# Kernel tuning notes

Measured on AMD Instinct MI355X. Metric: run time of the kernel, lower is better.

The kernel has to match this reference:

```python
import jax, jax.numpy as jnp
import numpy as np

IN_DIM = 128
OUT_DIM = 128
HEADS = 4
HEAD_DIM = OUT_DIM // HEADS
N_NODES = 50000
N_EDGES = 800000
NEG_SLOPE = 0.2
LN_EPS = 1e-5


def setup_inputs() -> dict:
    key = jax.random.key(0)
    ks = jax.random.split(key, 10)
    x = jax.random.normal(ks[0], (N_NODES, IN_DIM), dtype=jnp.float32)
    edge_index = jax.random.randint(ks[1], (2, N_EDGES), 0, N_NODES, dtype=jnp.int64)
    s = 1.0 / np.sqrt(IN_DIM)
    W_l = jax.random.normal(ks[2], (IN_DIM, HEADS * HEAD_DIM), dtype=jnp.float32) * s
    b_l = jnp.zeros((HEADS * HEAD_DIM,), dtype=jnp.float32)
    W_r = jax.random.normal(ks[3], (IN_DIM, HEADS * HEAD_DIM), dtype=jnp.float32) * s
    b_r = jnp.zeros((HEADS * HEAD_DIM,), dtype=jnp.float32)
    att = jax.random.normal(ks[4], (HEADS, HEAD_DIM), dtype=jnp.float32) * (1.0 / np.sqrt(HEAD_DIM))
    bias = jnp.zeros((HEADS * HEAD_DIM,), dtype=jnp.float32)
    gamma = jnp.ones((OUT_DIM,), dtype=jnp.float32)
    beta = jnp.zeros((OUT_DIM,), dtype=jnp.float32)
    return {"x": x, "edge_index": edge_index, "W_l": W_l, "b_l": b_l,
            "W_r": W_r, "b_r": b_r, "att": att, "bias": bias,
            "gamma": gamma, "beta": beta}


def reference(x, edge_index, W_l, b_l, W_r, b_r, att, bias, gamma, beta):
    N = x.shape[0]
    src, dst = edge_index[0], edge_index[1]
    # GATv2: separate linear transforms for source and target nodes
    xl = (x @ W_l + b_l).reshape(N, HEADS, HEAD_DIM)  # source / message features
    xr = (x @ W_r + b_r).reshape(N, HEADS, HEAD_DIM)  # target features
    # per-edge attention logits: a^T . leaky_relu(xl[src] + xr[dst])  -> [E, H]
    h = jax.nn.leaky_relu(xl[src] + xr[dst], NEG_SLOPE)
    e = jnp.einsum('ehd,hd->eh', h, att)
    # segment softmax over edges grouped by destination node
    m = jax.ops.segment_max(e, dst, num_segments=N)
    m = jnp.where(jnp.isfinite(m), m, 0.0)  # guard empty segments
    ex = jnp.exp(e - m[dst])
    denom = jax.ops.segment_sum(ex, dst, num_segments=N)
    alpha = ex / (denom[dst] + 1e-16)  # [E, H]
    # scatter-add weighted source features (dropout omitted: eval mode)
    out = jax.ops.segment_sum(alpha[:, :, None] * xl[src], dst, num_segments=N)
    out = out.reshape(N, HEADS * HEAD_DIM) + bias
    # residual (in_dim == out_dim) + LayerNorm
    out = out + x
    mu = out.mean(axis=-1, keepdims=True)
    var = ((out - mu) ** 2).mean(axis=-1, keepdims=True)
    return (out - mu) * jax.lax.rsqrt(var + LN_EPS) * gamma + beta
```

## Files before the change

kernel.cpp:

```cpp
#include <hip/hip_runtime.h>
#include <math.h>

#define NEG_SLOPE 0.2f
#define LN_EPS 1e-5f
#define CAP 64
#define HB 4096
#define RUN 56
#define XSTR 136
#define SMEM_BYTES (64 * XSTR * 2)

typedef __attribute__((ext_vector_type(8))) short s8v;
typedef __attribute__((ext_vector_type(8))) unsigned short u8v;
typedef __attribute__((ext_vector_type(4))) float f4v;
typedef _Float16 h2 __attribute__((ext_vector_type(2)));

__device__ inline unsigned short f2bf(float f) {
    unsigned u = __float_as_uint(f);
    return (unsigned short)((u + 0x7FFFu + ((u >> 16) & 1u)) >> 16);
}
__device__ inline unsigned cvt_pk_bf16(float lo, float hi) {
    unsigned r;
    asm("v_cvt_pk_bf16_f32 %0, %1, %2" : "=v"(r) : "v"(lo), "v"(hi));
    return r;
}

__global__ __launch_bounds__(256) void pre_scat_kernel(
    const int* __restrict__ src, const int* __restrict__ dst,
    const float* __restrict__ Wl, const float* __restrict__ Wr,
    unsigned short* __restrict__ packL, unsigned short* __restrict__ packR,
    unsigned* __restrict__ part, int* __restrict__ cntmat,
    int E, int NBKT) {
    const int bid = blockIdx.x, tid = threadIdx.x;
    if (bid < 2) {
        const float* W = bid ? Wr : Wl;
        unsigned short* pk = bid ? packR : packL;
        #pragma unroll
        for (int it = 0; it < 16; ++it) {
            int pos4 = tid + it * 256;
            int k = pos4 >> 5, c4 = pos4 & 31;
            float4 v = *(const float4*)&W[k * 128 + c4 * 4];
            int t = k >> 5, lane_hi = (k & 31) >> 3, j = k & 7;
            float vv[4] = {v.x, v.y, v.z, v.w};
            #pragma unroll
            for (int u = 0; u < 4; ++u) {
                int n = c4 * 4 + u;
                int idx = ((((n >> 4) * 4 + t) * 64) + lane_hi * 16 + (n & 15)) * 8 + j;
                pk[idx] = f2bf(vv[u]);
            }
        }
        return;
    }
    __shared__ int cnt[256];
    const int sb = bid - 2;
    const int e0 = sb * HB;
    cnt[tid] = 0;
    __syncthreads();
    for (int j = tid; j < HB; j += 256) {
        int e = e0 + j;
        if (e < E) {
            int d = dst[e];
            int b = d >> 8;
            int r = atomicAdd(&cnt[b], 1);
            if (r < RUN)
                part[((size_t)sb * NBKT + b) * RUN + r] =
                    ((unsigned)(d & 255) << 16) | (unsigned)src[e];
        }
    }
    __syncthreads();
    if (tid < NBKT) {
        int c = cnt[tid]; if (c > RUN) c = RUN;
        cntmat[(size_t)sb * NBKT + tid] = c;
    }
}

__global__ __launch_bounds__(256, 4) void fill_tf_kernel(
    const unsigned* __restrict__ part, const int* __restrict__ cntmat,
    unsigned short* __restrict__ csr, int* __restrict__ deg,
    const float* __restrict__ x,
    const unsigned short* __restrict__ packL, const unsigned short* __restrict__ packR,
    const float* __restrict__ bl, const float* __restrict__ br,
    _Float16* __restrict__ xl, _Float16* __restrict__ xr,
    int N, int NBKT, int NSC) {
    const int bid = blockIdx.x, tid = threadIdx.x;
    __shared__ __align__(16) char smem[SMEM_BYTES];

    if (bid < NBKT) {
        int* cur = (int*)smem;
        cur[tid] = 0;
        __syncthreads();
        const int b = bid;
        if (tid < NSC) {
            int cnt = cntmat[(size_t)tid * NBKT + b];
            const unsigned* seg = part + ((size_t)tid * NBKT + b) * RUN;
            for (int i = 0; i < cnt; ++i) {
                unsigned rec = seg[i];
                int dl = rec >> 16;
                int pos = atomicAdd(&cur[dl], 1);
                if (pos < CAP)
                    csr[(size_t)(b * 256 + dl) * CAP + (((pos & 3) << 4) | (pos >> 2))] =
                        (unsigned short)(rec & 0xFFFFu);
            }
        }
        __syncthreads();
        int node = b * 256 + tid;
        if (node < N) deg[node] = cur[tid];
        return;
    }

    const int tb = bid - NBKT;
    const int blk0 = tb * 64;
    const int wv = tid >> 6, lane = tid & 63;
    const int row = lane & 15, q = lane >> 4;
    const int nrow = blk0 + wv * 16 + row;
    const bool rowok = nrow < N;

    s8v afrag[4];
    {
        const float* xrow = &x[(size_t)nrow * 128];
        #pragma unroll
        for (int t = 0; t < 4; ++t) {
            float4 va = make_float4(0.f, 0.f, 0.f, 0.f);
            float4 vb = make_float4(0.f, 0.f, 0.f, 0.f);
            if (rowok) {
                va = *(const float4*)&xrow[t * 32 + q * 8];
                vb = *(const float4*)&xrow[t * 32 + q * 8 + 4];
            }
            union { unsigned u[4]; s8v v; } cv;
            cv.u[0] = cvt_pk_bf16(va.x, va.y);
            cv.u[1] = cvt_pk_bf16(va.z, va.w);
            cv.u[2] = cvt_pk_bf16(vb.x, vb.y);
            cv.u[3] = cvt_pk_bf16(vb.z, vb.w);
            afrag[t] = cv.v;
        }
    }

    _Float16* ys = (_Float16*)smem;

    #pragma unroll 1
    for (int side = 0; side < 2; ++side) {
        const unsigned short* __restrict__ pk = side ? packR : packL;
        const float* __restrict__ bb = side ? br : bl;
        _Float16* __restrict__ dsth = side ? xr : xl;

        f4v acc[8];
        #pragma unroll
        for (int nt = 0; nt < 8; ++nt) acc[nt] = (f4v){0.f, 0.f, 0.f, 0.f};

        #pragma unroll
        for (int t = 0; t < 4; ++t) {
            #pragma unroll
            for (int np = 0; np < 2; ++np) {
                s8v bfr[4];
                #pragma unroll
                for (int u = 0; u < 4; ++u)
                    bfr[u] = *(const s8v*)&pk[(((np * 4 + u) * 4 + t) * 64 + lane) * 8];
                #pragma unroll
                for (int u = 0; u < 4; ++u)
                    acc[np * 4 + u] = __builtin_amdgcn_mfma_f32_16x16x32_bf16(
                        afrag[t], bfr[u], acc[np * 4 + u], 0, 0, 0);
            }
        }

        #pragma unroll
        for (int nt = 0; nt < 8; ++nt) {
            float bcol = bb[nt * 16 + row];
            #pragma unroll
            for (int r2 = 0; r2 < 4; ++r2)
                ys[(wv * 16 + q * 4 + r2) * XSTR + nt * 16 + row] =
                    (_Float16)(acc[nt][r2] + bcol);
        }
        __syncthreads();
        #pragma unroll
        for (int it = 0; it < 4; ++it) {
            int slot = tid + it * 256;
            int rrow = slot >> 4, c8 = slot & 15;
            int nd = blk0 + rrow;
            if (nd < N)
                *(float4*)&dsth[(size_t)nd * 128 + c8 * 8] =
                    *(const float4*)&ys[rrow * XSTR + c8 * 8];
        }
        __syncthreads();
    }
}

__device__ inline void edge_body(float4 raw, const h2* xr2, const h2* av2,
                                 h2 ns2, float& den, float* acc) {
    h2 c[4];
    c[0] = __builtin_bit_cast(h2, raw.x);
    c[1] = __builtin_bit_cast(h2, raw.y);
    c[2] = __builtin_bit_cast(h2, raw.z);
    c[3] = __builtin_bit_cast(h2, raw.w);
    float p = 0.f;
    #pragma unroll
    for (int j = 0; j < 4; ++j) {
        h2 t = c[j] + xr2[j];
        h2 hh = __builtin_elementwise_max(t, t * ns2);
#if __has_builtin(__builtin_amdgcn_fdot2)
        p = __builtin_amdgcn_fdot2(hh, av2[j], p, false);
#else
        p = fmaf((float)hh.x, (float)av2[j].x, p);
        p = fmaf((float)hh.y, (float)av2[j].y, p);
#endif
    }
    p += __shfl_xor(p, 1);
    p += __shfl_xor(p, 2);
    float w = __expf(p);
    den += w;
    #pragma unroll
    for (int j = 0; j < 4; ++j) {
        acc[2 * j]     = fmaf(w, (float)c[j].x, acc[2 * j]);
        acc[2 * j + 1] = fmaf(w, (float)c[j].y, acc[2 * j + 1]);
    }
}

__global__ __launch_bounds__(256) void gat_kernel(
    const int* __restrict__ deg_arr, const unsigned short* __restrict__ csr,
    const _Float16* __restrict__ xl, const _Float16* __restrict__ xr,
    const float* __restrict__ att, const float* __restrict__ x,
    const float* __restrict__ bias, const float* __restrict__ gamma,
    const float* __restrict__ beta, float* __restrict__ out, int N) {
    const int node = blockIdx.x * 4 + (threadIdx.x >> 6);
    const int lane = threadIdx.x & 63;
    if (node >= N) return;
    const int sub = lane & 15;
    const int eg  = lane >> 4;
    const int f0  = sub * 8;

    int dg = deg_arr[node]; if (dg > CAP) dg = CAP;
    const unsigned short* crow = csr + (size_t)node * CAP;
    u8v cidx = *(const u8v*)&crow[eg * 16];

    h2 xr2[4], av2[4];
    {
        float4 xrw = *(const float4*)&xr[(size_t)node * 128 + f0];
        float fw[4]; fw[0] = xrw.x; fw[1] = xrw.y; fw[2] = xrw.z; fw[3] = xrw.w;
        #pragma unroll
        for (int j = 0; j < 4; ++j) xr2[j] = __builtin_bit_cast(h2, fw[j]);
        float4 c0 = *(const float4*)&att[f0];
        float4 c1 = *(const float4*)&att[f0 + 4];
        av2[0] = (h2){(_Float16)c0.x, (_Float16)c0.y};
        av2[1] = (h2){(_Float16)c0.z, (_Float16)c0.w};
        av2[2] = (h2){(_Float16)c1.x, (_Float16)c1.y};
        av2[3] = (h2){(_Float16)c1.z, (_Float16)c1.w};
    }
    const h2 ns2 = (h2){(_Float16)NEG_SLOPE, (_Float16)NEG_SLOPE};

    float4 bufv[8];
    #pragma unroll
    for (int k = 0; k < 8; ++k) {
        int i = eg + 4 * k;
        if (i < dg) bufv[k] = *(const float4*)&xl[(size_t)(unsigned short)cidx[k] * 128 + f0];
    }

    float den0 = 0.f, den1 = 0.f;
    float a0[8] = {0,0,0,0,0,0,0,0}, a1[8] = {0,0,0,0,0,0,0,0};

    #pragma unroll
    for (int k = 0; k < 8; k += 2) {
        if (eg + 4 * k < dg)       edge_body(bufv[k],     xr2, av2, ns2, den0, a0);
        if (eg + 4 * (k + 1) < dg) edge_body(bufv[k + 1], xr2, av2, ns2, den1, a1);
    }

    if (dg > 32) {
        u8v cidx2 = *(const u8v*)&crow[eg * 16 + 8];
        #pragma unroll
        for (int k = 0; k < 8; ++k) {
            int i = eg + 32 + 4 * k;
            if (i < dg) {
                float4 raw = *(const float4*)&xl[(size_t)(unsigned short)cidx2[k] * 128 + f0];
                edge_body(raw, xr2, av2, ns2, (k & 1) ? den1 : den0, (k & 1) ? a1 : a0);
            }
        }
    }

    float den = den0 + den1;
    float acc[8];
    #pragma unroll
    for (int j = 0; j < 8; ++j) acc[j] = a0[j] + a1[j];

    den += __shfl_xor(den, 16); den += __shfl_xor(den, 32);
    #pragma unroll
    for (int j = 0; j < 8; ++j) {
        acc[j] += __shfl_xor(acc[j], 16);
        acc[j] += __shfl_xor(acc[j], 32);
    }

    const float inv = 1.0f / (den + 1e-16f);
    float v[8];
    {
        float4 b0 = *(const float4*)&bias[f0];
        float4 b1 = *(const float4*)&bias[f0 + 4];
        float4 r0 = *(const float4*)&x[(size_t)node * 128 + f0];
        float4 r1 = *(const float4*)&x[(size_t)node * 128 + f0 + 4];
        const float bbf[8] = {b0.x, b0.y, b0.z, b0.w, b1.x, b1.y, b1.z, b1.w};
        const float rrf[8] = {r0.x, r0.y, r0.z, r0.w, r1.x, r1.y, r1.z, r1.w};
        #pragma unroll
        for (int j = 0; j < 8; ++j) v[j] = acc[j] * inv + bbf[j] + rrf[j];
    }

    float s = v[0] + v[1] + v[2] + v[3] + v[4] + v[5] + v[6] + v[7];
    s += __shfl_xor(s, 1); s += __shfl_xor(s, 2);
    s += __shfl_xor(s, 4); s += __shfl_xor(s, 8);
    const float mu = s * (1.0f / 128.0f);

    float d[8], vs = 0.f;
    #pragma unroll
    for (int j = 0; j < 8; ++j) { d[j] = v[j] - mu; vs = fmaf(d[j], d[j], vs); }
    vs += __shfl_xor(vs, 1); vs += __shfl_xor(vs, 2);
    vs += __shfl_xor(vs, 4); vs += __shfl_xor(vs, 8);
    const float rstd = rsqrtf(vs * (1.0f / 128.0f) + LN_EPS);

    if (eg == 0) {
        float4 g0 = *(const float4*)&gamma[f0];
        float4 g1 = *(const float4*)&gamma[f0 + 4];
        float4 e0 = *(const float4*)&beta[f0];
        float4 e1 = *(const float4*)&beta[f0 + 4];
        float4 o0, o1;
        o0.x = d[0] * rstd * g0.x + e0.x;  o0.y = d[1] * rstd * g0.y + e0.y;
        o0.z = d[2] * rstd * g0.z + e0.z;  o0.w = d[3] * rstd * g0.w + e0.w;
        o1.x = d[4] * rstd * g1.x + e1.x;  o1.y = d[5] * rstd * g1.y + e1.y;
        o1.z = d[6] * rstd * g1.z + e1.z;  o1.w = d[7] * rstd * g1.w + e1.w;
        *(float4*)&out[(size_t)node * 128 + f0]     = o0;
        *(float4*)&out[(size_t)node * 128 + f0 + 4] = o1;
    }
}

extern "C" void kernel_launch(void* const* d_in, const int* in_sizes, int n_in,
                              void* d_out, int out_size, void* d_ws, size_t ws_size,
                              hipStream_t stream) {
    const float* x     = (const float*)d_in[0];
    const int*   ei    = (const int*)d_in[1];
    const float* Wl    = (const float*)d_in[2];
    const float* bl    = (const float*)d_in[3];
    const float* Wr    = (const float*)d_in[4];
    const float* br    = (const float*)d_in[5];
    const float* att   = (const float*)d_in[6];
    const float* bias  = (const float*)d_in[7];
    const float* gamma = (const float*)d_in[8];
    const float* beta  = (const float*)d_in[9];

    const int N = in_sizes[0] / 128;
    const int E = in_sizes[1] / 2;
    const int* src = ei;
    const int* dst = ei + E;

    const int NBKT = (N + 255) >> 8;
    const int NSC  = (E + HB - 1) / HB;
    const int TBS  = (N + 63) / 64;

    char* w = (char*)d_ws;
    _Float16*       xl    = (_Float16*)w;        w += (size_t)N * 128 * sizeof(_Float16);
    _Float16*       xr    = (_Float16*)w;        w += (size_t)N * 128 * sizeof(_Float16);
    unsigned short* packL = (unsigned short*)w;  w += 16384 * sizeof(unsigned short);
    unsigned short* packR = (unsigned short*)w;  w += 16384 * sizeof(unsigned short);
    unsigned*       part  = (unsigned*)w;        w += (size_t)NSC * NBKT * RUN * sizeof(unsigned);
    int*            cntmat= (int*)w;             w += (size_t)NSC * NBKT * sizeof(int);
    unsigned short* csr   = (unsigned short*)w;  w += (size_t)N * CAP * sizeof(unsigned short);
    int*            deg   = (int*)w;             w += (size_t)N * sizeof(int);

    pre_scat_kernel<<<2 + NSC, 256, 0, stream>>>(
        src, dst, Wl, Wr, packL, packR, part, cntmat, E, NBKT);
    fill_tf_kernel<<<NBKT + TBS, 256, 0, stream>>>(
        part, cntmat, csr, deg, x, packL, packR, bl, br, xl, xr, N, NBKT, NSC);
    gat_kernel<<<(N + 3) / 4, 256, 0, stream>>>(
        deg, csr, xl, xr, att, x, bias, gamma, beta, (float*)d_out, N);
}
```

Before: 160.5 us.

## Merge edge scatter into fill/transform kernel with global-flag inter-block sync

The edge-bucketing scatter moves out of the first kernel and into the combined fill/transform kernel. Scatter blocks bump a global counter when they finish, and CSR-fill blocks spin on that counter before reading the partitions. The linear-transform blocks do not depend on the scatter, so they can overlap with it and one kernel-boundary drain goes away. Weight packing stays in a tiny separate kernel that also resets the flag. The risks are a deadlock if the waiting blocks become resident before the scatter blocks get scheduled, and spin overhead; launch bounds also rise to 5 waves per SIMD.

After: 243.3 us. +51.6%, slower.

```diff
diff --git a/kernel.cpp b/kernel.cpp
--- a/kernel.cpp
+++ b/kernel.cpp
@@ -24,71 +24,87 @@
     return r;
 }
 
-__global__ __launch_bounds__(256) void pre_scat_kernel(
-    const int* __restrict__ src, const int* __restrict__ dst,
+__global__ __launch_bounds__(256) void pre_kernel(
     const float* __restrict__ Wl, const float* __restrict__ Wr,
     unsigned short* __restrict__ packL, unsigned short* __restrict__ packR,
+    int* __restrict__ flags) {
+    const int bid = blockIdx.x, tid = threadIdx.x;
+    if (bid == 2) {
+        if (tid == 0) flags[0] = 0;
+        return;
+    }
+    const float* W = bid ? Wr : Wl;
+    unsigned short* pk = bid ? packR : packL;
+    #pragma unroll
+    for (int it = 0; it < 16; ++it) {
+        int pos4 = tid + it * 256;
+        int k = pos4 >> 5, c4 = pos4 & 31;
+        float4 v = *(const float4*)&W[k * 128 + c4 * 4];
+        int t = k >> 5, lane_hi = (k & 31) >> 3, j = k & 7;
+        float vv[4] = {v.x, v.y, v.z, v.w};
+        #pragma unroll
+        for (int u = 0; u < 4; ++u) {
+            int n = c4 * 4 + u;
+            int idx = ((((n >> 4) * 4 + t) * 64) + lane_hi * 16 + (n & 15)) * 8 + j;
+            pk[idx] = f2bf(vv[u]);
+        }
+    }
+}
+
+__global__ __launch_bounds__(256, 5) void scat_fill_tf_kernel(
+    const int* __restrict__ src, const int* __restrict__ dst,
     unsigned* __restrict__ part, int* __restrict__ cntmat,
-    int E, int NBKT) {
-    const int bid = blockIdx.x, tid = threadIdx.x;
-    if (bid < 2) {
-        const float* W = bid ? Wr : Wl;
-        unsigned short* pk = bid ? packR : packL;
-        #pragma unroll
-        for (int it = 0; it < 16; ++it) {
-            int pos4 = tid + it * 256;
-            int k = pos4 >> 5, c4 = pos4 & 31;
-            float4 v = *(const float4*)&W[k * 128 + c4 * 4];
-            int t = k >> 5, lane_hi = (k & 31) >> 3, j = k & 7;
-            float vv[4] = {v.x, v.y, v.z, v.w};
-            #pragma unroll
-            for (int u = 0; u < 4; ++u) {
-                int n = c4 * 4 + u;
-                int idx = ((((n >> 4) * 4 + t) * 64) + lane_hi * 16 + (n & 15)) * 8 + j;
-                pk[idx] = f2bf(vv[u]);
-            }
-        }
-        return;
-    }
-    __shared__ int cnt[256];
-    const int sb = bid - 2;
-    const int e0 = sb * HB;
-    cnt[tid] = 0;
-    __syncthreads();
-    for (int j = tid; j < HB; j += 256) {
-        int e = e0 + j;
-        if (e < E) {
-            int d = dst[e];
-            int b = d >> 8;
-            int r = atomicAdd(&cnt[b], 1);
-            if (r < RUN)
-                part[((size_t)sb * NBKT + b) * RUN + r] =
-                    ((unsigned)(d & 255) << 16) | (unsigned)src[e];
-        }
-    }
-    __syncthreads();
-    if (tid < NBKT) {
-        int c = cnt[tid]; if (c > RUN) c = RUN;
-        cntmat[(size_t)sb * NBKT + tid] = c;
-    }
-}
-
-__global__ __launch_bounds__(256, 4) void fill_tf_kernel(
-    const unsigned* __restrict__ part, const int* __restrict__ cntmat,
     unsigned short* __restrict__ csr, int* __restrict__ deg,
     const float* __restrict__ x,
     const unsigned short* __restrict__ packL, const unsigned short* __restrict__ packR,
     const float* __restrict__ bl, const float* __restrict__ br,
     _Float16* __restrict__ xl, _Float16* __restrict__ xr,
-    int N, int NBKT, int NSC) {
+    int* __restrict__ flags,
+    int N, int E, int NBKT, int NSC) {
     const int bid = blockIdx.x, tid = threadIdx.x;
     __shared__ __align__(16) char smem[SMEM_BYTES];
 
-    if (bid < NBKT) {
+    if (bid < NSC) {
+        int* cnt = (int*)smem;
+        const int sb = bid;
+        const int e0 = sb * HB;
+        cnt[tid] = 0;
+        __syncthreads();
+        for (int j = tid; j < HB; j += 256) {
+            int e = e0 + j;
+            if (e < E) {
+                int d = dst[e];
+                int b = d >> 8;
+                int r = atomicAdd(&cnt[b], 1);
+                if (r < RUN)
+                    part[((size_t)sb * NBKT + b) * RUN + r] =
+                        ((unsigned)(d & 255) << 16) | (unsigned)src[e];
+            }
+        }
+        __syncthreads();
+        if (tid < NBKT) {
+            int c = cnt[tid]; if (c > RUN) c = RUN;
+            cntmat[(size_t)sb * NBKT + tid] = c;
+        }
+        __syncthreads();
+        if (tid == 0) {
+            __threadfence();
+            __hip_atomic_fetch_add(&flags[0], 1, __ATOMIC_RELEASE, __HIP_MEMORY_SCOPE_AGENT);
+        }
+        return;
+    }
+
+    if (bid < NSC + NBKT) {
+        if (tid == 0) {
+            while (__hip_atomic_load(&flags[0], __ATOMIC_ACQUIRE, __HIP_MEMORY_SCOPE_AGENT) < NSC)
+                __builtin_amdgcn_s_sleep(16);
+            __threadfence();
+        }
+        __syncthreads();
         int* cur = (int*)smem;
         cur[tid] = 0;
         __syncthreads();
-        const int b = bid;
+        const int b = bid - NSC;
         if (tid < NSC) {
             int cnt = cntmat[(size_t)tid * NBKT + b];
             const unsigned* seg = part + ((size_t)tid * NBKT + b) * RUN;
@@ -107,7 +123,7 @@
         return;
     }
 
-    const int tb = bid - NBKT;
+    const int tb = bid - NSC - NBKT;
     const int blk0 = tb * 64;
     const int wv = tid >> 6, lane = tid & 63;
     const int row = lane & 15, q = lane >> 4;
@@ -357,11 +373,12 @@
     int*            cntmat= (int*)w;             w += (size_t)NSC * NBKT * sizeof(int);
     unsigned short* csr   = (unsigned short*)w;  w += (size_t)N * CAP * sizeof(unsigned short);
     int*            deg   = (int*)w;             w += (size_t)N * sizeof(int);
-
-    pre_scat_kernel<<<2 + NSC, 256, 0, stream>>>(
-        src, dst, Wl, Wr, packL, packR, part, cntmat, E, NBKT);
-    fill_tf_kernel<<<NBKT + TBS, 256, 0, stream>>>(
-        part, cntmat, csr, deg, x, packL, packR, bl, br, xl, xr, N, NBKT, NSC);
+    int*            flags = (int*)w;             w += 64;
+
+    pre_kernel<<<3, 256, 0, stream>>>(Wl, Wr, packL, packR, flags);
+    scat_fill_tf_kernel<<<NSC + NBKT + TBS, 256, 0, stream>>>(
+        src, dst, part, cntmat, csr, deg, x, packL, packR, bl, br, xl, xr,
+        flags, N, E, NBKT, NSC);
     gat_kernel<<<(N + 3) / 4, 256, 0, stream>>>(
         deg, csr, xl, xr, att, x, bias, gamma, beta, (float*)d_out, N);
 }
```
